# Kernel optimization log

Hardware: AMD Instinct MI355X
Metric: run time of the kernel (lower is better)

The kernel has to match this reference:

```python
import jax, jax.numpy as jnp
import numpy as np

B, HS, NS = 4096, 4, 64          # batch, hedge_size, neighbor_samples
T = 32                            # n_types (type_dim == output_dim)
E = 64                            # nodeEmb feature width
N_NODES, N_HEDGES = 100000, 500000


def setup_inputs() -> dict:
    key = jax.random.key(0)
    ks = jax.random.split(key, 8)
    return {
        "neighbors": jax.random.randint(ks[0], (B, HS), 0, N_NODES, dtype=jnp.int64)
            if jax.config.jax_enable_x64 else jax.random.randint(ks[0], (B, HS), 0, N_NODES).astype(jnp.int32),
        "train_hedges": jax.random.randint(ks[1], (B,), 0, N_HEDGES).astype(jnp.int32),
        "labels": jax.random.randint(ks[2], (B,), 0, T).astype(jnp.int32),
        "neighborhedges": jax.random.randint(ks[3], (N_NODES, NS), 0, N_HEDGES).astype(jnp.int32),
        "hedgetypes": jax.random.randint(ks[4], (N_HEDGES,), 0, T).astype(jnp.int32),
        "nodeEmb": jax.random.randint(ks[5], (N_NODES, E), 0, 100).astype(jnp.int32),
        "type_features": jnp.eye(T, dtype=jnp.float32),  # _build_type_feature: identity one-hot table
        "W1": jax.random.normal(ks[6], (T, T), dtype=jnp.float32) * 0.1,
        "b1": jnp.zeros((T,), dtype=jnp.float32),
        "W2": jax.random.normal(ks[7], (E, T), dtype=jnp.float32) * 0.1,
        "b2": jnp.zeros((T,), dtype=jnp.float32),
    }


def reference(neighbors, train_hedges, labels, neighborhedges, hedgetypes, nodeEmb,
              type_features, W1, b1, W2, b2):
    b, hs = neighbors.shape
    ns = neighborhedges.shape[1]
    # _get_neighbors_and_masks: chained gathers
    flat_nodes = neighbors.reshape(-1)
    neighbor_edges = neighborhedges[flat_nodes].reshape(b, hs * ns)      # [B, HS*NS]
    node_emb = nodeEmb[flat_nodes].reshape(b, hs, -1).astype(jnp.float32)  # [B, HS, E]
    mask = (neighbor_edges != train_hedges[:, None]).astype(jnp.float32)  # exclude training hyperedge
    # _aggregate_neighbors: gather types then one-hot type features
    self_vec = type_features[labels]                                      # [B, T]
    types = hedgetypes[neighbor_edges.reshape(-1)]                        # [B*HS*NS]
    nv = type_features[types].reshape(b, hs, ns, -1)                      # [B, HS, NS, T]
    m = mask.reshape(b, hs, ns, 1)
    # MeanAggregator (PathCon-style): masked mean over samples, mean over hedge slots,
    # add self vector, linear layer (identity activation; scores feed CrossEntropyLoss)
    avg = (nv * m).sum(axis=-2) / jnp.maximum(m.sum(axis=-2), 1.0)        # [B, HS, T]
    agg = avg.mean(axis=1) + self_vec                                     # [B, T]
    vector1 = agg @ W1 + b1                                               # [B, T] == scores
    node_feat = node_emb.mean(axis=1) @ W2 + b2                           # [B, T]
    embedding = jnp.concatenate([vector1, node_feat], axis=-1)            # [B, 2T]
    scores = vector1
    scores_normalized = jax.nn.sigmoid(scores)
    return scores, scores_normalized, embedding
```

## Files before the change

### kernel.cpp

```cpp
#include <hip/hip_runtime.h>
#include <hip/hip_bf16.h>

constexpr int HS = 4;
constexpr int NS = 64;
constexpr int T  = 32;
constexpr int E  = 64;

__global__ __launch_bounds__(256)
void polyhype_kernel(const int*   __restrict__ neighbors,
                     const int*   __restrict__ train_hedges,
                     const int*   __restrict__ labels,
                     const int*   __restrict__ neighborhedges,
                     const int*   __restrict__ hedgetypes,
                     const int*   __restrict__ nodeEmb,
                     const float* __restrict__ tf,
                     const float* __restrict__ W1,
                     const float* __restrict__ b1,
                     const float* __restrict__ W2,
                     const float* __restrict__ b2,
                     float*       __restrict__ out,
                     int B)
{
    const int b    = blockIdx.x;
    const int wid  = threadIdx.x >> 6;
    const int lane = threadIdx.x & 63;
    const int t    = lane & 31;

    __shared__ float aggp[HS][T];
    __shared__ float embp[HS][E];
    __shared__ float emb_mean[E];
    __shared__ float agg_full[T];

    const int th   = train_hedges[b];
    const int node = neighbors[b * HS + wid];

    const int edge = neighborhedges[(size_t)node * NS + lane];
    const int ty   = hedgetypes[edge];
    embp[wid][lane] = (float)nodeEmb[(size_t)node * E + lane];

    const unsigned long long mm = __ballot(edge != th);
    const float rden = 1.0f / fmaxf((float)__popcll(mm), 1.0f);

    float s = 0.f;
    #pragma unroll
    for (int k = 0; k < T; ++k) {
        const float cnt = (float)__popcll(__ballot(ty == k) & mm);
        s += cnt * tf[k * T + t];
    }
    if (lane < T) aggp[wid][t] = s * rden;

    __syncthreads();

    if (wid == 0) {
        if (lane < T) {
            float agg = (aggp[0][t] + aggp[1][t] + aggp[2][t] + aggp[3][t]) * 0.25f
                      + tf[labels[b] * T + t];
            agg_full[t] = agg;
        }
        __builtin_amdgcn_wave_barrier();
        if (lane < T) {
            float v = b1[t];
            #pragma unroll 8
            for (int u = 0; u < T; ++u)
                v += agg_full[u] * W1[u * T + t];
            float* scores = out;
            float* sig    = out + (size_t)B * T;
            float* emb    = out + (size_t)2 * B * T;
            scores[b * T + t] = v;
            sig[b * T + t]    = 1.0f / (1.0f + __expf(-v));
            emb[(size_t)b * 2 * T + t] = v;
        }
    } else if (wid == 1) {
        emb_mean[lane] = (embp[0][lane] + embp[1][lane] + embp[2][lane] + embp[3][lane]) * 0.25f;
        __builtin_amdgcn_wave_barrier();
        if (lane < T) {
            float v = b2[t];
            #pragma unroll 8
            for (int e = 0; e < E; ++e)
                v += emb_mean[e] * W2[e * T + t];
            float* emb = out + (size_t)2 * B * T;
            emb[(size_t)b * 2 * T + T + t] = v;
        }
    }
}

extern "C" void kernel_launch(void* const* d_in, const int* in_sizes, int n_in,
                              void* d_out, int out_size, void* d_ws, size_t ws_size,
                              hipStream_t stream) {
    const int*   neighbors      = (const int*)  d_in[0];
    const int*   train_hedges   = (const int*)  d_in[1];
    const int*   labels         = (const int*)  d_in[2];
    const int*   neighborhedges = (const int*)  d_in[3];
    const int*   hedgetypes     = (const int*)  d_in[4];
    const int*   nodeEmb        = (const int*)  d_in[5];
    const float* tf             = (const float*)d_in[6];
    const float* W1             = (const float*)d_in[7];
    const float* b1             = (const float*)d_in[8];
    const float* W2             = (const float*)d_in[9];
    const float* b2             = (const float*)d_in[10];
    float*       out            = (float*)      d_out;

    const int B = in_sizes[1];

    polyhype_kernel<<<B, 256, 0, stream>>>(
        neighbors, train_hedges, labels, neighborhedges, hedgetypes, nodeEmb,
        tf, W1, b1, W2, b2, out, B);
}
```

Before: 17.04 us.

## Process two batch rows per block and spread epilogue across all waves

Each 256-thread block now handles two batch rows, which halves the grid size and lets each wave issue two independent gather chains, increasing memory-level parallelism. The epilogue work for scores and node features is now split across all four waves, where before only two were used, and shared scratch buffers are reused in place. The cost is more registers per thread, plus an unguarded second row that assumes B is even.

New measurement: 17.00 us. Within noise of the previous version (-0.2%).

```diff
diff --git a/kernel.cpp b/kernel.cpp
--- a/kernel.cpp
+++ b/kernel.cpp
@@ -5,6 +5,7 @@
 constexpr int NS = 64;
 constexpr int T  = 32;
 constexpr int E  = 64;
+constexpr int RPB = 2;
 
 __global__ __launch_bounds__(256)
 void polyhype_kernel(const int*   __restrict__ neighbors,
@@ -21,65 +22,81 @@
                      float*       __restrict__ out,
                      int B)
 {
-    const int b    = blockIdx.x;
     const int wid  = threadIdx.x >> 6;
     const int lane = threadIdx.x & 63;
     const int t    = lane & 31;
+    const int b0   = blockIdx.x * RPB;
+    const int b1r  = b0 + 1;
 
-    __shared__ float aggp[HS][T];
-    __shared__ float embp[HS][E];
-    __shared__ float emb_mean[E];
-    __shared__ float agg_full[T];
+    __shared__ float aggp[RPB][HS][T];
+    __shared__ float embp[RPB][HS][E];
 
-    const int th   = train_hedges[b];
-    const int node = neighbors[b * HS + wid];
+    const int th0 = train_hedges[b0];
+    const int th1 = train_hedges[b1r];
+    const int n0  = neighbors[b0  * HS + wid];
+    const int n1  = neighbors[b1r * HS + wid];
 
-    const int edge = neighborhedges[(size_t)node * NS + lane];
-    const int ty   = hedgetypes[edge];
-    embp[wid][lane] = (float)nodeEmb[(size_t)node * E + lane];
+    const int e0 = neighborhedges[(size_t)n0 * NS + lane];
+    const int e1 = neighborhedges[(size_t)n1 * NS + lane];
+    const int t0 = hedgetypes[e0];
+    const int t1 = hedgetypes[e1];
+    embp[0][wid][lane] = (float)nodeEmb[(size_t)n0 * E + lane];
+    embp[1][wid][lane] = (float)nodeEmb[(size_t)n1 * E + lane];
 
-    const unsigned long long mm = __ballot(edge != th);
-    const float rden = 1.0f / fmaxf((float)__popcll(mm), 1.0f);
+    const unsigned long long mm0 = __ballot(e0 != th0);
+    const unsigned long long mm1 = __ballot(e1 != th1);
+    const float rd0 = 1.0f / fmaxf((float)__popcll(mm0), 1.0f);
+    const float rd1 = 1.0f / fmaxf((float)__popcll(mm1), 1.0f);
 
-    float s = 0.f;
+    float s0 = 0.f, s1 = 0.f;
     #pragma unroll
     for (int k = 0; k < T; ++k) {
-        const float cnt = (float)__popcll(__ballot(ty == k) & mm);
-        s += cnt * tf[k * T + t];
+        const float w  = tf[k * T + t];
+        const float c0 = (float)__popcll(__ballot(t0 == k) & mm0);
+        const float c1 = (float)__popcll(__ballot(t1 == k) & mm1);
+        s0 += c0 * w;
+        s1 += c1 * w;
     }
-    if (lane < T) aggp[wid][t] = s * rden;
+    if (lane < T) {
+        aggp[0][wid][t] = s0 * rd0;
+        aggp[1][wid][t] = s1 * rd1;
+    }
 
     __syncthreads();
 
-    if (wid == 0) {
+    const int r  = wid >> 1;
+    const int br = b0 + r;
+    float* scores = out;
+    float* sig    = out + (size_t)B * T;
+    float* emb    = out + (size_t)2 * B * T;
+
+    if ((wid & 1) == 0) {
         if (lane < T) {
-            float agg = (aggp[0][t] + aggp[1][t] + aggp[2][t] + aggp[3][t]) * 0.25f
-                      + tf[labels[b] * T + t];
-            agg_full[t] = agg;
+            float agg = (aggp[r][0][t] + aggp[r][1][t] + aggp[r][2][t] + aggp[r][3][t]) * 0.25f
+                      + tf[labels[br] * T + t];
+            aggp[r][0][t] = agg;
         }
         __builtin_amdgcn_wave_barrier();
         if (lane < T) {
             float v = b1[t];
             #pragma unroll 8
             for (int u = 0; u < T; ++u)
-                v += agg_full[u] * W1[u * T + t];
-            float* scores = out;
-            float* sig    = out + (size_t)B * T;
-            float* emb    = out + (size_t)2 * B * T;
-            scores[b * T + t] = v;
-            sig[b * T + t]    = 1.0f / (1.0f + __expf(-v));
-            emb[(size_t)b * 2 * T + t] = v;
+                v += aggp[r][0][u] * W1[u * T + t];
+            scores[br * T + t] = v;
+            sig[br * T + t]    = 1.0f / (1.0f + __expf(-v));
+            emb[(size_t)br * 2 * T + t] = v;
         }
-    } else if (wid == 1) {
-        emb_mean[lane] = (embp[0][lane] + embp[1][lane] + embp[2][lane] + embp[3][lane]) * 0.25f;
+    } else {
+        const float em = (embp[r][0][lane] + embp[r][1][lane] +
+                          embp[r][2][lane] + embp[r][3][lane]) * 0.25f;
+        embp[r][0][lane] = em;
         __builtin_amdgcn_wave_barrier();
         if (lane < T) {
             float v = b2[t];
             #pragma unroll 8
             for (int e = 0; e < E; ++e)
-                v += emb_mean[e] * W2[e * T + t];
-            float* emb = out + (size_t)2 * B * T;
-            emb[(size_t)b * 2 * T + T + t] = v;
+                v += embp[r][0][e] * W2[e * T + t];
+            emb[(size_t)br * 2 * T + T + t] = v;
         }
     }
 }
@@ -102,7 +119,8 @@
 
     const int B = in_sizes[1];
 
-    polyhype_kernel<<<B, 256, 0, stream>>>(
+    const int grid = (B + RPB - 1) / RPB;
+    polyhype_kernel<<<grid, 256, 0, stream>>>(
         neighbors, train_hedges, labels, neighborhedges, hedgetypes, nodeEmb,
         tf, W1, b1, W2, b2, out, B);
 }
```
